# Optimization experiments

Hardware: AMD Instinct MI355X
Metric: run time of the kernel (lower is better)

## Reference

```python
import jax, jax.numpy as jnp
import numpy as np

B, N_BOX, N_THING, ROI = 2, 32, 4, 28
H, W = 768, 704
N_STUFF = 6
N_CLS = N_STUFF + N_THING  # 10
NEG = -100.0


def setup_inputs() -> dict:
    key = jax.random.key(0)
    k1, k2, k3, k4 = jax.random.split(key, 4)
    sem_logits = jax.random.normal(k1, (B, N_CLS, H, W), jnp.float32)
    roi_msk_logits = jax.random.normal(k2, (B, N_BOX, N_THING, ROI, ROI), jnp.float32)
    cls = jax.random.randint(k3, (B, N_BOX), 0, N_THING, jnp.int32)
    u = jax.random.uniform(k4, (B, N_BOX, 4), jnp.float32)
    y0 = u[..., 0] * (H - 80.0)
    x0 = u[..., 1] * (W - 80.0)
    y1 = jnp.minimum(y0 + 32.0 + u[..., 2] * (H / 3.0), H - 1.0)
    x1 = jnp.minimum(x0 + 32.0 + u[..., 3] * (W / 3.0), W - 1.0)
    bbx = jnp.stack([y0, x0, y1, x1], axis=-1)  # (y_min, x_min, y_max, x_max)
    img_size = jnp.array([H, W], jnp.int32)
    return {"sem_logits": sem_logits, "roi_msk_logits": roi_msk_logits,
            "bbx": bbx, "cls": cls, "img_size": img_size}


def _bilinear_paste(msk, bbx, img_size, Hs, Ws):
    # msk: [B,N,R,R]; per-box bilinear resize (align_corners=False) to (h,w) and paste
    # into a [B,N,Hs,Ws] canvas filled with -100, clipped to the image.
    R = msk.shape[-1]
    ref = jnp.floor(bbx).astype(jnp.int32)  # torch .long()/int() truncation (boxes >= 0)
    y0, x0, y1, x1 = ref[..., 0], ref[..., 1], ref[..., 2], ref[..., 3]
    h = jnp.maximum(y1 - y0 + 1, 1).astype(jnp.float32)
    w = jnp.maximum(x1 - x0 + 1, 1).astype(jnp.float32)
    yy = jnp.arange(Hs, dtype=jnp.float32)[None, None, :]          # [1,1,H]
    sy = jnp.clip((yy - y0[..., None] + 0.5) * (R / h)[..., None] - 0.5, 0.0, R - 1.0)
    ylo = jnp.floor(sy).astype(jnp.int32)
    yhi = jnp.minimum(ylo + 1, R - 1)
    wy = sy - ylo                                                   # [B,N,H]
    xx = jnp.arange(Ws, dtype=jnp.float32)[None, None, :]
    sx = jnp.clip((xx - x0[..., None] + 0.5) * (R / w)[..., None] - 0.5, 0.0, R - 1.0)
    xlo = jnp.floor(sx).astype(jnp.int32)
    xhi = jnp.minimum(xlo + 1, R - 1)
    wx = sx - xlo                                                   # [B,N,W]
    rows = (jnp.take_along_axis(msk, ylo[..., None], axis=2) * (1.0 - wy[..., None])
            + jnp.take_along_axis(msk, yhi[..., None], axis=2) * wy[..., None])  # [B,N,H,R]
    up = (jnp.take_along_axis(rows, xlo[:, :, None, :], axis=3) * (1.0 - wx[:, :, None, :])
          + jnp.take_along_axis(rows, xhi[:, :, None, :], axis=3) * wx[:, :, None, :])  # [B,N,H,W]
    yi = jnp.arange(Hs, dtype=jnp.int32)[None, None, :]
    xi = jnp.arange(Ws, dtype=jnp.int32)[None, None, :]
    in_y = (yi >= jnp.maximum(y0, 0)[..., None]) & (yi < jnp.minimum(y1 + 1, img_size[0])[..., None])
    in_x = (xi >= jnp.maximum(x0, 0)[..., None]) & (xi < jnp.minimum(x1 + 1, img_size[1])[..., None])
    inside = in_y[..., :, None] & in_x[..., None, :]
    return jnp.where(inside, up, NEG)


def _fused_logits(sem_logits, roi_msk_logits, bbx, cls, img_size):
    Bs, _, Hs, Ws = sem_logits.shape
    Nb = cls.shape[1]
    # gather per-box mask logits for its predicted thing class: [B,N,R,R]
    msk = roi_msk_logits[jnp.arange(Bs)[:, None], jnp.arange(Nb)[None, :], cls]
    po_mask = _bilinear_paste(msk, bbx, img_size, Hs, Ws)          # [B,N,H,W]
    # semantic-logit crops per box (po_sem_stride = 1)
    iy0 = jnp.floor(bbx[..., 0]).astype(jnp.int32)
    ix0 = jnp.floor(bbx[..., 1]).astype(jnp.int32)
    iy1 = (jnp.round(bbx[..., 2]) + 1.0).astype(jnp.int32)
    ix1 = (jnp.round(bbx[..., 3]) + 1.0).astype(jnp.int32)
    yi = jnp.arange(Hs, dtype=jnp.int32)[None, None, :]
    xi = jnp.arange(Ws, dtype=jnp.int32)[None, None, :]
    in2 = (((yi >= iy0[..., None]) & (yi < iy1[..., None]))[..., :, None]
           & ((xi >= ix0[..., None]) & (xi < ix1[..., None]))[..., None, :])
    sem_sel = sem_logits[:, N_STUFF:][jnp.arange(Bs)[:, None], cls]  # [B,N,H,W]
    po_inst = jnp.where(in2, sem_sel, NEG)
    combined = (jax.nn.sigmoid(po_inst) + jax.nn.sigmoid(po_mask)) * (po_inst + po_mask)
    return jnp.concatenate([sem_logits[:, :N_STUFF], combined], axis=1)  # [B,6+N,H,W]


def _label_single(pp, sp, cl):
    # pp: panoptic argmax [H,W]; sp: semantic argmax [H,W]; cl: [N] thing classes
    Nb = cl.shape[0]
    is_inst = pp >= N_STUFF
    nmap = jnp.clip(pp - N_STUFF, 0, Nb - 1)
    # joint histogram counts[n, c] = #pixels with po_pred == 6+n and sem_pred == c
    key = jnp.where(is_inst, (pp - N_STUFF) * N_CLS + sp, Nb * N_CLS)
    counts = jnp.zeros(Nb * N_CLS + 1, jnp.int32).at[key.ravel()].add(1)[:Nb * N_CLS].reshape(Nb, N_CLS)
    present = counts.sum(1) > 0
    idx = jnp.cumsum(present.astype(jnp.int32)) - 1  # enumeration order of torch.unique ids
    maj = jnp.argmax(counts, axis=1).astype(jnp.int32)  # ties -> smallest class (matches unique+argmax)
    frac = counts.max(1).astype(jnp.float32) / jnp.maximum(counts.sum(1), 1).astype(jnp.float32)
    thing = cl.astype(jnp.int32) + N_STUFF
    match = maj == thing
    to_stuff = (~match) & (frac >= 0.5) & (maj < N_STUFF)
    sem_val = jnp.where(to_stuff, maj, thing)
    inst_val = jnp.where(to_stuff, -1, idx)
    po_sem = jnp.where(is_inst, sem_val[nmap], pp)
    po_inst = jnp.where(is_inst, inst_val[nmap], -1)
    # po_min_stuff_area = 0 (default) -> stuff-area filter is a no-op
    sh = jnp.zeros(N_STUFF + 1, jnp.int32).at[jnp.where(po_sem < N_STUFF, po_sem, N_STUFF).ravel()].add(1)[:N_STUFF]
    s_present = sh > 0
    s_rank = jnp.cumsum(s_present.astype(jnp.int32)) - 1
    n_stuff = s_present.astype(jnp.int32).sum()
    ih = jnp.zeros(Nb + 1, jnp.int32).at[jnp.where(po_inst >= 0, po_inst, Nb).ravel()].add(1)[:Nb]
    i_present = ih > 0
    i_rank = jnp.cumsum(i_present.astype(jnp.int32)) - 1
    seam = jnp.where((po_inst < 0) & (po_sem < N_STUFF),
                     1 + s_rank[jnp.clip(po_sem, 0, N_STUFF - 1)], 0)
    seam = jnp.where(po_inst >= 0, 1 + n_stuff + i_rank[jnp.clip(po_inst, 0, Nb - 1)], seam)
    L = 1 + N_STUFF + Nb  # fixed-size padded po_cls (torch version is variable-length)
    cls_out = jnp.full(L, 255, jnp.int32)
    cls_out = cls_out.at[jnp.where(s_present, 1 + s_rank, L)].set(
        jnp.arange(N_STUFF, dtype=jnp.int32), mode='drop')
    inst_sem = jnp.full(Nb, 255, jnp.int32).at[
        jnp.where(present & (~to_stuff), idx, Nb)].set(sem_val.astype(jnp.int32), mode='drop')
    cls_out = cls_out.at[jnp.where(i_present, 1 + n_stuff + i_rank, L)].set(inst_sem, mode='drop')
    return seam.astype(jnp.int32), cls_out, jnp.zeros(L, jnp.int32)


def reference(sem_logits, roi_msk_logits, bbx, cls, img_size):
    logits = _fused_logits(sem_logits, roi_msk_logits, bbx, cls, img_size)
    po_pred = jnp.argmax(logits, axis=1)        # softmax is monotone -> argmax of logits
    sem_pred = jnp.argmax(sem_logits, axis=1)
    seam, po_cls, po_iscrowd = jax.vmap(_label_single)(po_pred, sem_pred, cls)
    Bs, Hs, Ws = seam.shape
    return seam.reshape(Bs * Hs, Ws), po_cls.reshape(-1), po_iscrowd.reshape(-1)
```

## Files before the change

kernel.cpp:

```cpp
#include <hip/hip_runtime.h>
#include <math.h>

#define NSTUFF 6
#define NCLS   10
#define NBOX   32
#define NTHING 4
#define RR     28
#define HH     768
#define WW     704
#define NPIX   (HH * WW)
#define BB     2
#define LL     (1 + NSTUFF + NBOX)
#define NEGV   (-100.0f)

#define TW 64
#define TH 16
#define TILES_X (WW / TW)
#define TILES_Y (HH / TH)
#define NTILES  (TILES_X * TILES_Y)
#define NHIST   (NBOX * NCLS + NSTUFF)

__device__ __forceinline__ float sigmoidf_(float x) {
    return 1.0f / (1.0f + expf(-x));
}

__global__ __launch_bounds__(256) void k_fuse(
    const float* __restrict__ sem,
    const float* __restrict__ roi,
    const float* __restrict__ bbx,
    const int*   __restrict__ cls,
    uchar4*      __restrict__ pred8,
    int*         __restrict__ counts,
    int*         __restrict__ stuffh)
{
    const int b = blockIdx.y;
    __shared__ int   sh_y0[NBOX], sh_x0[NBOX], sh_yme[NBOX], sh_xme[NBOX];
    __shared__ int   sh_yie[NBOX], sh_xie[NBOX], sh_moff[NBOX], sh_cls[NBOX];
    __shared__ float sh_y0f[NBOX], sh_x0f[NBOX], sh_sy[NBOX], sh_sx[NBOX];
    __shared__ int   sh_list[NBOX];
    __shared__ int   sh_nbox;
    __shared__ int   sh_cnt[NHIST];

    const int t = threadIdx.x;
    const int tile = blockIdx.x;
    const int tx0 = (tile % TILES_X) * TW;
    const int ty0 = (tile / TILES_X) * TH;

    const int xq = tx0 + (t & 15) * 4;
    const int y  = ty0 + (t >> 4);
    const int p  = y * WW + xq;

    const float* semb = sem + (size_t)b * NCLS * NPIX;
    float4 s4[NCLS];
    #pragma unroll
    for (int c = 0; c < NCLS; ++c)
        s4[c] = *(const float4*)(semb + (size_t)c * NPIX + p);

    for (int i = t; i < NHIST; i += 256) sh_cnt[i] = 0;

    if (t < 64) {
        bool flag = false;
        if (t < NBOX) {
            const float* bbp = bbx + ((size_t)b * NBOX + t) * 4;
            float y0f = bbp[0], x0f = bbp[1], y1f = bbp[2], x1f = bbp[3];
            int y0 = (int)floorf(y0f), x0 = (int)floorf(x0f);
            int y1 = (int)floorf(y1f), x1 = (int)floorf(x1f);
            int yme = min(y1 + 1, HH), xme = min(x1 + 1, WW);
            int yie = (int)rintf(y1f) + 1, xie = (int)rintf(x1f) + 1;
            sh_y0[t] = y0;  sh_x0[t] = x0;
            sh_yme[t] = yme; sh_xme[t] = xme;
            sh_yie[t] = yie; sh_xie[t] = xie;
            sh_y0f[t] = (float)y0; sh_x0f[t] = (float)x0;
            float hh = (float)max(y1 - y0 + 1, 1);
            float ww = (float)max(x1 - x0 + 1, 1);
            sh_sy[t] = 28.0f / hh;  sh_sx[t] = 28.0f / ww;
            int c = cls[b * NBOX + t];
            sh_cls[t] = c;
            sh_moff[t] = (((b * NBOX + t) * NTHING) + c) * (RR * RR);
            int uy = max(yme, yie), ux = max(xme, xie);
            flag = (y0 < ty0 + TH) && (uy > ty0) && (x0 < tx0 + TW) && (ux > tx0);
        }
        unsigned long long m = __ballot(flag);
        if (flag) {
            int pos = __popcll(m & (((unsigned long long)1 << t) - 1ull));
            sh_list[pos] = t;
        }
        if (t == 0) sh_nbox = __popcll(m);
    }
    __syncthreads();

    const int nb = sh_nbox;

    auto doPix = [&](const float* s, int y_, int x_, int& bi_o, int& sp_o) {
        const float yf = (float)y_, xf = (float)x_;
        float sb = s[0]; int sp = 0;
        #pragma unroll
        for (int c = 1; c < NCLS; ++c) if (s[c] > sb) { sb = s[c]; sp = c; }

        float bv = s[0]; int bi = 0;
        #pragma unroll
        for (int c = 1; c < NSTUFF; ++c) if (s[c] > bv) { bv = s[c]; bi = c; }

        int prev = -1;
        for (int j = 0; j < nb; ++j) {
            const int n = sh_list[j];
            if (n > prev + 1 && bv < 0.0f) { bv = -0.0f; bi = NSTUFF + prev + 1; }
            const bool in_m = (y_ >= max(sh_y0[n], 0)) & (y_ < sh_yme[n]) &
                              (x_ >= max(sh_x0[n], 0)) & (x_ < sh_xme[n]);
            const bool in_i = (y_ >= sh_y0[n]) & (y_ < sh_yie[n]) &
                              (x_ >= sh_x0[n]) & (x_ < sh_xie[n]);
            float v;
            if (in_m | in_i) {
                float pm = NEGV;
                if (in_m) {
                    float sy = __fsub_rn(__fmul_rn(__fadd_rn(__fsub_rn(yf, sh_y0f[n]), 0.5f), sh_sy[n]), 0.5f);
                    sy = fminf(fmaxf(sy, 0.0f), 27.0f);
                    int ylo = (int)sy;
                    int yhi = min(ylo + 1, RR - 1);
                    float wy = __fsub_rn(sy, (float)ylo);
                    float sx = __fsub_rn(__fmul_rn(__fadd_rn(__fsub_rn(xf, sh_x0f[n]), 0.5f), sh_sx[n]), 0.5f);
                    sx = fminf(fmaxf(sx, 0.0f), 27.0f);
                    int xlo = (int)sx;
                    int xhi = min(xlo + 1, RR - 1);
                    float wx = __fsub_rn(sx, (float)xlo);
                    const float* m = roi + sh_moff[n];
                    float m00 = m[ylo * RR + xlo], m01 = m[ylo * RR + xhi];
                    float m10 = m[yhi * RR + xlo], m11 = m[yhi * RR + xhi];
                    float omy = __fsub_rn(1.0f, wy), omx = __fsub_rn(1.0f, wx);
                    float rl = __fadd_rn(__fmul_rn(m00, omy), __fmul_rn(m10, wy));
                    float rh = __fadd_rn(__fmul_rn(m01, omy), __fmul_rn(m11, wy));
                    pm = __fadd_rn(__fmul_rn(rl, omx), __fmul_rn(rh, wx));
                }
                float pi = NEGV;
                if (in_i) {
                    int c = sh_cls[n];
                    pi = (c == 0) ? s[6] : (c == 1) ? s[7] : (c == 2) ? s[8] : s[9];
                }
                v = __fmul_rn(__fadd_rn(sigmoidf_(pi), sigmoidf_(pm)), __fadd_rn(pi, pm));
            } else {
                v = -0.0f;
            }
            if (v > bv) { bv = v; bi = NSTUFF + n; }
            prev = n;
        }
        if (prev < NBOX - 1 && bv < 0.0f) { bi = NSTUFF + prev + 1; }
        bi_o = bi; sp_o = sp;
    };

    int bis[4], sps[4];
    #pragma unroll
    for (int j = 0; j < 4; ++j) {
        float s[NCLS];
        #pragma unroll
        for (int c = 0; c < NCLS; ++c) s[c] = ((const float*)&s4[c])[j];
        doPix(s, y, xq + j, bis[j], sps[j]);
    }

    uchar4 pv;
    pv.x = (unsigned char)bis[0]; pv.y = (unsigned char)bis[1];
    pv.z = (unsigned char)bis[2]; pv.w = (unsigned char)bis[3];
    pred8[((size_t)b * NPIX + p) >> 2] = pv;

    const int lane = t & 63;
    #pragma unroll
    for (int s = 0; s < NSTUFF; ++s) {
        int c = 0;
        #pragma unroll
        for (int j = 0; j < 4; ++j) c += __popcll(__ballot(bis[j] == s));
        if (lane == 0 && c) atomicAdd(&sh_cnt[NBOX * NCLS + s], c);
    }
    #pragma unroll
    for (int j = 0; j < 4; ++j)
        if (bis[j] >= NSTUFF) atomicAdd(&sh_cnt[(bis[j] - NSTUFF) * NCLS + sps[j]], 1);

    __syncthreads();
    for (int i = t; i < NHIST; i += 256) {
        int v = sh_cnt[i];
        if (v) {
            if (i < NBOX * NCLS) atomicAdd(&counts[b * NBOX * NCLS + i], v);
            else                 atomicAdd(&stuffh[b * NSTUFF + (i - NBOX * NCLS)], v);
        }
    }
}

__global__ __launch_bounds__(256) void k_relabel(
    const int*    __restrict__ counts,
    const int*    __restrict__ stuffh,
    const int*    __restrict__ cls,
    const uchar4* __restrict__ pred8,
    int*          __restrict__ out)
{
    const int b = blockIdx.y;
    const int t = threadIdx.x;
    __shared__ int slut[NSTUFF + NBOX];
    __shared__ int l_sh[NSTUFF];
    __shared__ int l_ih[NBOX];
    __shared__ int l_isem[NBOX];
    __shared__ int l_co[LL];

    const size_t q = (size_t)b * (NPIX / 4) + (size_t)blockIdx.x * 256 + t;
    const uchar4 v = pred8[q];

    int  ssum = 0, mj = 0, semv = 0, idx = -1;
    bool pres = false, ts = false;

    if (t < 64) {
        if (t < NSTUFF) l_sh[t] = stuffh[b * NSTUFF + t];
        if (t < NBOX)  { l_ih[t] = 0; l_isem[t] = 255; }
        if (t < LL)      l_co[t] = 255;

        if (t < NBOX) {
            const int* C = counts + ((size_t)b * NBOX + t) * NCLS;
            int c[NCLS];
            #pragma unroll
            for (int i = 0; i < NCLS; ++i) c[i] = C[i];
            int m = c[0]; mj = 0; ssum = c[0];
            #pragma unroll
            for (int i = 1; i < NCLS; ++i) {
                ssum += c[i];
                if (c[i] > m) { m = c[i]; mj = i; }
            }
            pres = ssum > 0;
            int thing = cls[b * NBOX + t] + NSTUFF;
            ts = pres && (mj != thing) && (2 * m >= ssum) && (mj < NSTUFF);
            semv = ts ? mj : thing;
        }
        unsigned long long pm = __ballot(pres);
        idx = __popcll(pm & (((unsigned long long)2 << t) - 1ull)) - 1;

        if (t < NBOX && pres &&  ts) atomicAdd(&l_sh[mj], ssum);
        if (t < NBOX && pres && !ts) { atomicAdd(&l_ih[idx], ssum); l_isem[idx] = semv; }
    }
    __syncthreads();

    if (t < 64) {
        bool spres = (t < NSTUFF) && (l_sh[t] > 0);
        unsigned long long sm = __ballot(spres);
        const int nst = __popcll(sm);
        bool ipres = (t < NBOX) && (l_ih[t] > 0);
        unsigned long long im = __ballot(ipres);

        auto srank = [&](int c) { return __popcll(sm & (((unsigned long long)2 << c) - 1ull)) - 1; };
        auto irank = [&](int j) { return __popcll(im & (((unsigned long long)2 << j) - 1ull)) - 1; };

        if (t < NSTUFF) slut[t] = 1 + srank(t);
        if (t < NBOX) {
            int q2 = idx < 0 ? 0 : idx;
            slut[NSTUFF + t] = ts ? (1 + srank(mj)) : (1 + nst + irank(q2));
        }
        if (spres) l_co[1 + srank(t)] = t;
        if (ipres) l_co[1 + nst + irank(t)] = l_isem[t];
    }
    __syncthreads();

    int4 o;
    o.x = slut[v.x];
    o.y = slut[v.y];
    o.z = slut[v.z];
    o.w = slut[v.w];
    ((int4*)out)[q] = o;

    if (blockIdx.x == 0 && t < LL) {
        int* ocls = out + (size_t)BB * NPIX + b * LL;
        int* ocrd = out + (size_t)BB * NPIX + BB * LL + b * LL;
        ocls[t] = l_co[t];
        ocrd[t] = 0;
    }
}

extern "C" void kernel_launch(void* const* d_in, const int* in_sizes, int n_in,
                              void* d_out, int out_size, void* d_ws, size_t ws_size,
                              hipStream_t stream) {
    (void)in_sizes; (void)n_in; (void)out_size; (void)ws_size;
    const float* sem = (const float*)d_in[0];
    const float* roi = (const float*)d_in[1];
    const float* bbx = (const float*)d_in[2];
    const int*   cls = (const int*)d_in[3];
    int* out = (int*)d_out;

    int* counts = (int*)d_ws;
    int* stuffh = counts + BB * NBOX * NCLS;
    uchar4* pred8 = (uchar4*)(stuffh + BB * NSTUFF);

    hipMemsetAsync(d_ws, 0, (BB * NBOX * NCLS + BB * NSTUFF) * sizeof(int), stream);

    dim3 g1(NTILES, BB);
    k_fuse<<<g1, 256, 0, stream>>>(sem, roi, bbx, cls, pred8, counts, stuffh);
    dim3 g2(NPIX / 1024, BB);
    k_relabel<<<g2, 256, 0, stream>>>(counts, stuffh, cls, pred8, out);
}
```

Baseline: 108.6 us.

## Interchange box and pixel loops, pack box params into vector LDS structs

Restructures the fusion kernel so the box loop is outermost and the four pixels per thread are processed inside it. This lets per-box row work (y interpolation, row pointers, class channel select) be computed once per box instead of once per pixel. Box parameters are packed into int4/float4 shared arrays so each box needs fewer LDS reads. The semantic logit loads are moved after the box setup, and the stuff argmax is reused as the start of the full argmax. The cost is more live registers for four parallel bv/bi/sp states.

```diff
diff --git a/kernel.cpp b/kernel.cpp
--- a/kernel.cpp
+++ b/kernel.cpp
@@ -34,9 +34,9 @@
     int*         __restrict__ stuffh)
 {
     const int b = blockIdx.y;
-    __shared__ int   sh_y0[NBOX], sh_x0[NBOX], sh_yme[NBOX], sh_xme[NBOX];
-    __shared__ int   sh_yie[NBOX], sh_xie[NBOX], sh_moff[NBOX], sh_cls[NBOX];
-    __shared__ float sh_y0f[NBOX], sh_x0f[NBOX], sh_sy[NBOX], sh_sx[NBOX];
+    __shared__ int4   sbA[NBOX];
+    __shared__ int4   sbB[NBOX];
+    __shared__ float4 sbF[NBOX];
     __shared__ int   sh_list[NBOX];
     __shared__ int   sh_nbox;
     __shared__ int   sh_cnt[NHIST];
@@ -49,14 +49,6 @@
     const int xq = tx0 + (t & 15) * 4;
     const int y  = ty0 + (t >> 4);
     const int p  = y * WW + xq;
-
-    const float* semb = sem + (size_t)b * NCLS * NPIX;
-    float4 s4[NCLS];
-    #pragma unroll
-    for (int c = 0; c < NCLS; ++c)
-        s4[c] = *(const float4*)(semb + (size_t)c * NPIX + p);
-
-    for (int i = t; i < NHIST; i += 256) sh_cnt[i] = 0;
 
     if (t < 64) {
         bool flag = false;
@@ -67,16 +59,12 @@
             int y1 = (int)floorf(y1f), x1 = (int)floorf(x1f);
             int yme = min(y1 + 1, HH), xme = min(x1 + 1, WW);
             int yie = (int)rintf(y1f) + 1, xie = (int)rintf(x1f) + 1;
-            sh_y0[t] = y0;  sh_x0[t] = x0;
-            sh_yme[t] = yme; sh_xme[t] = xme;
-            sh_yie[t] = yie; sh_xie[t] = xie;
-            sh_y0f[t] = (float)y0; sh_x0f[t] = (float)x0;
-            float hh = (float)max(y1 - y0 + 1, 1);
-            float ww = (float)max(x1 - x0 + 1, 1);
-            sh_sy[t] = 28.0f / hh;  sh_sx[t] = 28.0f / ww;
             int c = cls[b * NBOX + t];
-            sh_cls[t] = c;
-            sh_moff[t] = (((b * NBOX + t) * NTHING) + c) * (RR * RR);
+            sbA[t] = make_int4(y0, x0, yme, xme);
+            sbB[t] = make_int4(yie, xie, (((b * NBOX + t) * NTHING) + c) * (RR * RR), c);
+            float bh = (float)max(y1 - y0 + 1, 1);
+            float bw = (float)max(x1 - x0 + 1, 1);
+            sbF[t] = make_float4((float)y0, (float)x0, 28.0f / bh, 28.0f / bw);
             int uy = max(yme, yie), ux = max(xme, xie);
             flag = (y0 < ty0 + TH) && (uy > ty0) && (x0 < tx0 + TW) && (ux > tx0);
         }
@@ -87,78 +75,110 @@
         }
         if (t == 0) sh_nbox = __popcll(m);
     }
+
+    const float* semb = sem + (size_t)b * NCLS * NPIX;
+    float4 s4[NCLS];
+    #pragma unroll
+    for (int c = 0; c < NCLS; ++c)
+        s4[c] = *(const float4*)(semb + (size_t)c * NPIX + p);
+
+    for (int i = t; i < NHIST; i += 256) sh_cnt[i] = 0;
+
     __syncthreads();
 
     const int nb = sh_nbox;
-
-    auto doPix = [&](const float* s, int y_, int x_, int& bi_o, int& sp_o) {
-        const float yf = (float)y_, xf = (float)x_;
-        float sb = s[0]; int sp = 0;
+    const float yf = (float)y;
+
+    float bv[4]; int bi[4]; int sp[4];
+    #pragma unroll
+    for (int j = 0; j < 4; ++j) {
+        float m0 = ((const float*)&s4[0])[j]; int i0 = 0;
         #pragma unroll
-        for (int c = 1; c < NCLS; ++c) if (s[c] > sb) { sb = s[c]; sp = c; }
-
-        float bv = s[0]; int bi = 0;
+        for (int c = 1; c < NSTUFF; ++c) {
+            float v = ((const float*)&s4[c])[j];
+            if (v > m0) { m0 = v; i0 = c; }
+        }
+        bv[j] = m0; bi[j] = i0;
+        float sb = m0; int spx = i0;
         #pragma unroll
-        for (int c = 1; c < NSTUFF; ++c) if (s[c] > bv) { bv = s[c]; bi = c; }
-
-        int prev = -1;
-        for (int j = 0; j < nb; ++j) {
-            const int n = sh_list[j];
-            if (n > prev + 1 && bv < 0.0f) { bv = -0.0f; bi = NSTUFF + prev + 1; }
-            const bool in_m = (y_ >= max(sh_y0[n], 0)) & (y_ < sh_yme[n]) &
-                              (x_ >= max(sh_x0[n], 0)) & (x_ < sh_xme[n]);
-            const bool in_i = (y_ >= sh_y0[n]) & (y_ < sh_yie[n]) &
-                              (x_ >= sh_x0[n]) & (x_ < sh_xie[n]);
-            float v;
-            if (in_m | in_i) {
-                float pm = NEGV;
-                if (in_m) {
-                    float sy = __fsub_rn(__fmul_rn(__fadd_rn(__fsub_rn(yf, sh_y0f[n]), 0.5f), sh_sy[n]), 0.5f);
-                    sy = fminf(fmaxf(sy, 0.0f), 27.0f);
-                    int ylo = (int)sy;
-                    int yhi = min(ylo + 1, RR - 1);
-                    float wy = __fsub_rn(sy, (float)ylo);
-                    float sx = __fsub_rn(__fmul_rn(__fadd_rn(__fsub_rn(xf, sh_x0f[n]), 0.5f), sh_sx[n]), 0.5f);
-                    sx = fminf(fmaxf(sx, 0.0f), 27.0f);
-                    int xlo = (int)sx;
-                    int xhi = min(xlo + 1, RR - 1);
-                    float wx = __fsub_rn(sx, (float)xlo);
-                    const float* m = roi + sh_moff[n];
-                    float m00 = m[ylo * RR + xlo], m01 = m[ylo * RR + xhi];
-                    float m10 = m[yhi * RR + xlo], m11 = m[yhi * RR + xhi];
-                    float omy = __fsub_rn(1.0f, wy), omx = __fsub_rn(1.0f, wx);
-                    float rl = __fadd_rn(__fmul_rn(m00, omy), __fmul_rn(m10, wy));
-                    float rh = __fadd_rn(__fmul_rn(m01, omy), __fmul_rn(m11, wy));
-                    pm = __fadd_rn(__fmul_rn(rl, omx), __fmul_rn(rh, wx));
+        for (int c = NSTUFF; c < NCLS; ++c) {
+            float v = ((const float*)&s4[c])[j];
+            if (v > sb) { sb = v; spx = c; }
+        }
+        sp[j] = spx;
+    }
+
+    int prev = -1;
+    for (int jb = 0; jb < nb; ++jb) {
+        const int n = sh_list[jb];
+        const int4 A  = sbA[n];
+        const int4 Bc = sbB[n];
+        const bool iny_m = (y >= max(A.x, 0)) & (y < A.z);
+        const bool iny_i = (y >= A.x) & (y < Bc.x);
+        const int firstIdx = NSTUFF + ((n > prev + 1) ? (prev + 1) : n);
+
+        if (!(iny_m | iny_i)) {
+            #pragma unroll
+            for (int j = 0; j < 4; ++j)
+                if (bv[j] < 0.0f) { bv[j] = -0.0f; bi[j] = firstIdx; }
+        } else {
+            const float4 F = sbF[n];
+            int ylo = 0, yhi = 0; float wy = 0.0f, omy = 1.0f;
+            if (iny_m) {
+                float sy = __fsub_rn(__fmul_rn(__fadd_rn(__fsub_rn(yf, F.x), 0.5f), F.z), 0.5f);
+                sy = fminf(fmaxf(sy, 0.0f), 27.0f);
+                ylo = (int)sy;
+                yhi = min(ylo + 1, RR - 1);
+                wy = __fsub_rn(sy, (float)ylo);
+                omy = __fsub_rn(1.0f, wy);
+            }
+            const float* mrow = roi + Bc.z;
+            const float* mlo = mrow + ylo * RR;
+            const float* mhi = mrow + yhi * RR;
+            const int c = Bc.w;
+            float4 pz = (c == 0) ? s4[6] : (c == 1) ? s4[7] : (c == 2) ? s4[8] : s4[9];
+            float pich[4] = {pz.x, pz.y, pz.z, pz.w};
+            const int xm_lo = max(A.y, 0);
+
+            #pragma unroll
+            for (int j = 0; j < 4; ++j) {
+                const int x = xq + j;
+                if (n > prev + 1 && bv[j] < 0.0f) { bv[j] = -0.0f; bi[j] = NSTUFF + prev + 1; }
+                const bool in_m = iny_m & (x >= xm_lo) & (x < A.w);
+                const bool in_i = iny_i & (x >= A.y) & (x < Bc.y);
+                if (in_m | in_i) {
+                    float pm = NEGV;
+                    if (in_m) {
+                        float xf = (float)x;
+                        float sx = __fsub_rn(__fmul_rn(__fadd_rn(__fsub_rn(xf, F.y), 0.5f), F.w), 0.5f);
+                        sx = fminf(fmaxf(sx, 0.0f), 27.0f);
+                        int xlo = (int)sx;
+                        int xhi = min(xlo + 1, RR - 1);
+                        float wx = __fsub_rn(sx, (float)xlo);
+                        float omx = __fsub_rn(1.0f, wx);
+                        float m00 = mlo[xlo], m01 = mlo[xhi];
+                        float m10 = mhi[xlo], m11 = mhi[xhi];
+                        float rl = __fadd_rn(__fmul_rn(m00, omy), __fmul_rn(m10, wy));
+                        float rh = __fadd_rn(__fmul_rn(m01, omy), __fmul_rn(m11, wy));
+                        pm = __fadd_rn(__fmul_rn(rl, omx), __fmul_rn(rh, wx));
+                    }
+                    float pi = in_i ? pich[j] : NEGV;
+                    float v = __fmul_rn(__fadd_rn(sigmoidf_(pi), sigmoidf_(pm)), __fadd_rn(pi, pm));
+                    if (v > bv[j]) { bv[j] = v; bi[j] = NSTUFF + n; }
+                } else {
+                    if (bv[j] < 0.0f) { bv[j] = -0.0f; bi[j] = firstIdx; }
                 }
-                float pi = NEGV;
-                if (in_i) {
-                    int c = sh_cls[n];
-                    pi = (c == 0) ? s[6] : (c == 1) ? s[7] : (c == 2) ? s[8] : s[9];
-                }
-                v = __fmul_rn(__fadd_rn(sigmoidf_(pi), sigmoidf_(pm)), __fadd_rn(pi, pm));
-            } else {
-                v = -0.0f;
             }
-            if (v > bv) { bv = v; bi = NSTUFF + n; }
-            prev = n;
-        }
-        if (prev < NBOX - 1 && bv < 0.0f) { bi = NSTUFF + prev + 1; }
-        bi_o = bi; sp_o = sp;
-    };
-
-    int bis[4], sps[4];
-    #pragma unroll
-    for (int j = 0; j < 4; ++j) {
-        float s[NCLS];
-        #pragma unroll
-        for (int c = 0; c < NCLS; ++c) s[c] = ((const float*)&s4[c])[j];
-        doPix(s, y, xq + j, bis[j], sps[j]);
-    }
+        }
+        prev = n;
+    }
+    #pragma unroll
+    for (int j = 0; j < 4; ++j)
+        if (prev < NBOX - 1 && bv[j] < 0.0f) bi[j] = NSTUFF + prev + 1;
 
     uchar4 pv;
-    pv.x = (unsigned char)bis[0]; pv.y = (unsigned char)bis[1];
-    pv.z = (unsigned char)bis[2]; pv.w = (unsigned char)bis[3];
+    pv.x = (unsigned char)bi[0]; pv.y = (unsigned char)bi[1];
+    pv.z = (unsigned char)bi[2]; pv.w = (unsigned char)bi[3];
     pred8[((size_t)b * NPIX + p) >> 2] = pv;
 
     const int lane = t & 63;
@@ -166,12 +186,12 @@
     for (int s = 0; s < NSTUFF; ++s) {
         int c = 0;
         #pragma unroll
-        for (int j = 0; j < 4; ++j) c += __popcll(__ballot(bis[j] == s));
+        for (int j = 0; j < 4; ++j) c += __popcll(__ballot(bi[j] == s));
         if (lane == 0 && c) atomicAdd(&sh_cnt[NBOX * NCLS + s], c);
     }
     #pragma unroll
     for (int j = 0; j < 4; ++j)
-        if (bis[j] >= NSTUFF) atomicAdd(&sh_cnt[(bis[j] - NSTUFF) * NCLS + sps[j]], 1);
+        if (bi[j] >= NSTUFF) atomicAdd(&sh_cnt[(bi[j] - NSTUFF) * NCLS + sp[j]], 1);
 
     __syncthreads();
     for (int i = t; i < NHIST; i += 256) {
```

Measured after the change: 124.7 us. +14.8%, slower.
